# Kernel optimization log

Hardware: AMD Instinct MI355X
Metric: run time of the kernel (lower is better)

## Reference

```python
import jax, jax.numpy as jnp
import numpy as np

B, T, N, F_IN, F_OUT = 8, 16, 512, 128, 64
NEG_INF = -9e15


def setup_inputs() -> dict:
    key = jax.random.key(0)
    k1, k2, k3, k4, k5 = jax.random.split(key, 5)
    x = jax.random.normal(k1, (B, T, N, F_IN), dtype=jnp.float32)
    # nn.Linear weights: FC_W [out, in], FC_a [1, 2*out], no bias
    W = jax.random.normal(k2, (F_OUT, F_IN), dtype=jnp.float32) * 0.05
    a = jax.random.normal(k3, (1, 2 * F_OUT), dtype=jnp.float32) * 0.05
    adj = jax.random.randint(k4, (N, N), 0, 2, dtype=jnp.int32)
    adj_we = jax.random.uniform(k5, (N, N), dtype=jnp.float32)
    return {"x": x, "W": W, "a": a, "adj": adj, "adj_we": adj_we}


def reference(x, W, a, adj, adj_we):
    fout = W.shape[0]
    # h = FC_W(input): [B,T,N,Fout]
    h = jnp.einsum("btnf,of->btno", x, W)
    # Additive GAT score decomposition: e[i,j] = LeakyReLU(a1.h_i + a2.h_j)
    # (equivalent to FC_a(cat([h_i, h_j])) without materializing [B,T,N,N,2F])
    a1 = a[0, :fout]
    a2 = a[0, fout:]
    src = jnp.einsum("btno,o->btn", h, a1)  # contribution of node i (repeated rows)
    dst = jnp.einsum("btno,o->btn", h, a2)  # contribution of node j (tiled rows)
    e = jax.nn.leaky_relu(src[..., :, None] + dst[..., None, :], negative_slope=0.01)
    # mask where adj <= 0, scale by edge weights, softmax over neighbors (dim=3)
    att = jnp.where(adj > 0, e, NEG_INF)
    att = att * adj_we
    att = jax.nn.softmax(att, axis=-1)
    # h_prime = attention @ h : [B,T,N,N] @ [B,T,N,Fout]
    return jnp.einsum("btij,btjo->btio", att, h)
```

## Files before the change

### kernel.cpp

```cpp
#include <hip/hip_runtime.h>
#include <hip/hip_bf16.h>

#define BTOT 128
#define NN   512
#define FIN  128
#define FOUT 64

typedef __attribute__((ext_vector_type(8))) short bf16x8;
typedef __attribute__((ext_vector_type(4))) float f32x4;

static __device__ inline ushort f2bf(float f) {
    __hip_bfloat16 h = __float2bfloat16(f);
    return *(ushort*)&h;
}
static __device__ inline float bf2f(ushort u) {
    uint v = (uint)u << 16;
    return __uint_as_float(v);
}

__global__ void k_prep(const float* __restrict__ W, const int* __restrict__ adj,
                       const float* __restrict__ we, ushort* __restrict__ Whi,
                       ushort* __restrict__ Wlo, ushort* __restrict__ cds) {
    int b = blockIdx.x;
    if (b >= 256) {
        int i = (b - 256) * 256 + threadIdx.x;
        float w = W[i];
        ushort hi = f2bf(w);
        Whi[i] = hi;
        Wlo[i] = f2bf(w - bf2f(hi));
        return;
    }
    int i = (b * 256 + threadIdx.x) * 4;
    int4   a4 = *(const int4*)&adj[i];
    float4 w4 = *(const float4*)&we[i];
    ushort o[4];
#pragma unroll
    for (int e = 0; e < 4; ++e) {
        bool  cn = ((const int*)&a4)[e] > 0;
        float w  = ((const float*)&w4)[e];
        if (cn) {
            uint ub = __float_as_uint(w * 1.44269504f);
            uint tt = ub + 0xFFFFu + ((ub >> 17) & 1u);
            o[e] = (ushort)(((tt >> 17) << 1) | 1u);
        } else {
            o[e] = (w > 0.f) ? (ushort)0 : (ushort)1;
        }
    }
    *(uint2*)&cds[i] = *(uint2*)&o[0];
}

__global__ void k_feat(const float* __restrict__ x, const ushort* __restrict__ Whi,
                       const ushort* __restrict__ Wlo, const float* __restrict__ a,
                       ushort* __restrict__ ht, float* __restrict__ srcv,
                       float* __restrict__ dstv) {
    const int t    = threadIdx.x;
    const int bid  = blockIdx.x;
    const int bt   = bid & 127;
    const int nt   = bid >> 7;
    const int wv   = t >> 6, lane = t & 63;
    const int r    = lane & 15;
    const int kc   = lane >> 4;
    const int n0   = nt * 64 + wv * 16;

    const float* xrow = x + ((long)bt * NN + n0 + r) * FIN;

    f32x4 acc[4] = {{0,0,0,0},{0,0,0,0},{0,0,0,0},{0,0,0,0}};

#pragma unroll
    for (int ks = 0; ks < 4; ++ks) {
        f32x4 xa = __builtin_nontemporal_load((const f32x4*)&xrow[ks * 32 + kc * 8]);
        f32x4 xb = __builtin_nontemporal_load((const f32x4*)&xrow[ks * 32 + kc * 8 + 4]);
        float xv[8] = {xa[0], xa[1], xa[2], xa[3], xb[0], xb[1], xb[2], xb[3]};
        bf16x8 Ahi, Alo;
#pragma unroll
        for (int e = 0; e < 8; ++e) {
            uint b = __float_as_uint(xv[e]);
            float hf = __uint_as_float(b & 0xFFFF0000u);
            Ahi[e] = (short)(b >> 16);
            float rr = xv[e] - hf;
            Alo[e] = (short)(__float_as_uint(rr) >> 16);
        }
#pragma unroll
        for (int g = 0; g < 4; ++g) {
            const int wo = (g * 16 + r) * FIN + ks * 32 + kc * 8;
            bf16x8 Bhi = *(const bf16x8*)&Whi[wo];
            bf16x8 Blo = *(const bf16x8*)&Wlo[wo];
            acc[g] = __builtin_amdgcn_mfma_f32_16x16x32_bf16(Ahi, Bhi, acc[g], 0, 0, 0);
            acc[g] = __builtin_amdgcn_mfma_f32_16x16x32_bf16(Alo, Bhi, acc[g], 0, 0, 0);
            acc[g] = __builtin_amdgcn_mfma_f32_16x16x32_bf16(Ahi, Blo, acc[g], 0, 0, 0);
        }
    }

    float a1g[4], a2g[4];
#pragma unroll
    for (int g = 0; g < 4; ++g) {
        a1g[g] = a[g * 16 + r];
        a2g[g] = a[FOUT + g * 16 + r];
    }
    f32x4 s1v = {0,0,0,0}, s2v = {0,0,0,0};
#pragma unroll
    for (int g = 0; g < 4; ++g)
#pragma unroll
        for (int reg = 0; reg < 4; ++reg) {
            s1v[reg] += acc[g][reg] * a1g[g];
            s2v[reg] += acc[g][reg] * a2g[g];
        }
#pragma unroll
    for (int off = 8; off; off >>= 1)
#pragma unroll
        for (int reg = 0; reg < 4; ++reg) {
            s1v[reg] += __shfl_down(s1v[reg], off, 16);
            s2v[reg] += __shfl_down(s2v[reg], off, 16);
        }
    if (r == 0) {
        float4 o1 = make_float4(s1v[0], s1v[1], s1v[2], s1v[3]);
        float4 o2 = make_float4(s2v[0], s2v[1], s2v[2], s2v[3]);
        *(float4*)&srcv[bt * NN + n0 + kc * 4] = o1;
        *(float4*)&dstv[bt * NN + n0 + kc * 4] = o2;
    }

#pragma unroll
    for (int g = 0; g < 4; ++g) {
        uint2 pk;
        pk.x = (uint)f2bf(acc[g][0]) | ((uint)f2bf(acc[g][1]) << 16);
        pk.y = (uint)f2bf(acc[g][2]) | ((uint)f2bf(acc[g][3]) << 16);
        *(uint2*)&ht[(long)bt * (FOUT * NN) + (g * 16 + r) * NN + n0 + kc * 4] = pk;
    }
}

static __device__ inline bf16x8 make_afrag(uint4 c, float4 d0, float4 d1, float si) {
    float dv[8] = {d0.x, d0.y, d0.z, d0.w, d1.x, d1.y, d1.z, d1.w};
    uint  cw[4] = {c.x, c.y, c.z, c.w};
    union { uint u[4]; bf16x8 v; } A;
#pragma unroll
    for (int q = 0; q < 4; ++q) {
        uint u = cw[q];
        float c0 = __uint_as_float((u << 16) & 0xFFFE0000u);
        float c1 = __uint_as_float(u & 0xFFFE0000u);
        float s0 = si + dv[2 * q],     lr0 = fmaxf(s0, 0.01f * s0);
        float s1 = si + dv[2 * q + 1], lr1 = fmaxf(s1, 0.01f * s1);
        float p0 = __builtin_amdgcn_exp2f(c0 * lr0);
        float p1 = __builtin_amdgcn_exp2f(c1 * lr1);
        p0 = (u & 1u)       ? p0 : 0.f;
        p1 = (u & 0x10000u) ? p1 : 0.f;
        A.u[q] = __builtin_amdgcn_perm(__float_as_uint(p1), __float_as_uint(p0),
                                       0x07060302u);
    }
    return A.v;
}

__global__ __launch_bounds__(256, 4)
void k_attn(const ushort* __restrict__ ht, const float* __restrict__ srcv,
            const float* __restrict__ dstv, const ushort* __restrict__ cds,
            float* __restrict__ out) {
    __shared__ ushort hs[64 * 256];
    __shared__ float dst_s[NN];

    const int t    = threadIdx.x;
    const int bid  = blockIdx.x;
    const int bt   = bid & 127;
    const int i0   = (bid >> 7) << 6;
    const int lane = t & 63;
    const int wv   = t >> 6;
    const int r16  = lane & 15;
    const int kc   = lane >> 4;
    const int koff = kc * 8;
    const int xr   = r16 & 7;

    const int ri = i0 + wv * 16 + r16;
    const float si = srcv[bt * NN + ri];
    const ushort* cdr = cds + ri * NN;
    const ushort* htb = ht + (long)bt * (FOUT * NN);

    for (int q = t; q < NN; q += 256) dst_s[q] = dstv[bt * NN + q];

    f32x4 ac0 = {0,0,0,0}, ac1 = {0,0,0,0}, ac2 = {0,0,0,0}, ac3 = {0,0,0,0},
          acd = {0,0,0,0};
    bf16x8 ones;
#pragma unroll
    for (int j = 0; j < 8; ++j) ones[j] = (short)0x3F80;

#pragma unroll
    for (int half = 0; half < 2; ++half) {
        const int jg = half * 256;

        uint4 cdv[8];
#pragma unroll
        for (int c = 0; c < 4; ++c) {
            cdv[2 * c]     = *(const uint4*)&cdr[jg + c * 64 + koff];
            cdv[2 * c + 1] = *(const uint4*)&cdr[jg + c * 64 + 32 + koff];
        }

        __syncthreads();
#pragma unroll
        for (int q = 0; q < 8; ++q) {
            int idx = q * 256 + t;
            int o = idx >> 5, c8 = idx & 31;
            float4 v = *(const float4*)&htb[(o << 9) + (half << 8) + (c8 << 3)];
            *(float4*)&hs[(o << 8) + ((c8 ^ (o & 7)) << 3)] = v;
        }
        __syncthreads();

#pragma unroll
        for (int jtl = 0; jtl < 4; ++jtl) {
            const int jgc = jg + jtl * 64;
            float4 d00 = *(float4*)&dst_s[jgc + koff];
            float4 d01 = *(float4*)&dst_s[jgc + koff + 4];
            float4 d10 = *(float4*)&dst_s[jgc + 32 + koff];
            float4 d11 = *(float4*)&dst_s[jgc + 32 + koff + 4];

            bf16x8 A0 = make_afrag(cdv[2 * jtl],     d00, d01, si);
            bf16x8 A1 = make_afrag(cdv[2 * jtl + 1], d10, d11, si);

#pragma unroll
            for (int s2 = 0; s2 < 2; ++s2) {
                bf16x8 A = s2 ? A1 : A0;
                const int c8v = jtl * 8 + s2 * 4 + kc;
                const int cs  = (c8v ^ xr) << 3;
                bf16x8 b0 = *(bf16x8*)&hs[(( 0 + r16) << 8) + cs];
                bf16x8 b1 = *(bf16x8*)&hs[((16 + r16) << 8) + cs];
                bf16x8 b2 = *(bf16x8*)&hs[((32 + r16) << 8) + cs];
                bf16x8 b3 = *(bf16x8*)&hs[((48 + r16) << 8) + cs];
                __builtin_amdgcn_s_setprio(1);
                ac0 = __builtin_amdgcn_mfma_f32_16x16x32_bf16(A, b0, ac0, 0, 0, 0);
                ac1 = __builtin_amdgcn_mfma_f32_16x16x32_bf16(A, b1, ac1, 0, 0, 0);
                ac2 = __builtin_amdgcn_mfma_f32_16x16x32_bf16(A, b2, ac2, 0, 0, 0);
                ac3 = __builtin_amdgcn_mfma_f32_16x16x32_bf16(A, b3, ac3, 0, 0, 0);
                acd = __builtin_amdgcn_mfma_f32_16x16x32_bf16(A, ones, acd, 0, 0, 0);
                __builtin_amdgcn_s_setprio(0);
            }
        }
    }

    float* ob = out + ((long)bt * NN + i0 + wv * 16) * FOUT;
#pragma unroll
    for (int reg = 0; reg < 4; ++reg) {
        float inv = 1.0f / acd[reg];
        const int rw = (kc * 4 + reg) * FOUT + r16;
        __builtin_nontemporal_store(ac0[reg] * inv, &ob[rw +  0]);
        __builtin_nontemporal_store(ac1[reg] * inv, &ob[rw + 16]);
        __builtin_nontemporal_store(ac2[reg] * inv, &ob[rw + 32]);
        __builtin_nontemporal_store(ac3[reg] * inv, &ob[rw + 48]);
    }
}

extern "C" void kernel_launch(void* const* d_in, const int* in_sizes, int n_in,
                              void* d_out, int out_size, void* d_ws, size_t ws_size,
                              hipStream_t stream) {
    const float* x      = (const float*)d_in[0];
    const float* W      = (const float*)d_in[1];
    const float* a      = (const float*)d_in[2];
    const int*   adj    = (const int*)d_in[3];
    const float* adj_we = (const float*)d_in[4];
    float* out = (float*)d_out;

    ushort* Whi  = (ushort*)d_ws;
    ushort* Wlo  = Whi + FOUT * FIN;
    ushort* ht   = Wlo + FOUT * FIN;
    float*  srcv = (float*)(ht + BTOT * FOUT * NN);
    float*  dstv = srcv + BTOT * NN;
    ushort* cdsw = (ushort*)(dstv + BTOT * NN);

    hipLaunchKernelGGL(k_prep, dim3(288), dim3(256), 0, stream,
                       W, adj, adj_we, Whi, Wlo, cdsw);
    hipLaunchKernelGGL(k_feat, dim3(1024), dim3(256), 0, stream,
                       x, Whi, Wlo, a, ht, srcv, dstv);
    hipLaunchKernelGGL(k_attn, dim3(1024), dim3(256), 0, stream,
                       ht, srcv, dstv, cdsw, out);
}
```

Before: 48.36 us.

## Read attention B operands directly from global memory instead of LDS staging

Removes the shared-memory staging of the transposed h tile, along with its two barriers per half. Each wave now loads its MFMA B fragments straight from global or L2, and the cds row fragments are software-prefetched one chunk ahead. Launch bounds rise to 5 blocks per CU, since LDS use drops to just the dst vector. The trade-off is that the four waves of a block now fetch the same h data redundantly through cache instead of sharing it via LDS, and load latency is exposed directly on the MFMA path.

Result: slower. 70.88 us (+46.6%).

```diff
diff --git a/kernel.cpp b/kernel.cpp
--- a/kernel.cpp
+++ b/kernel.cpp
@@ -149,11 +149,10 @@
     return A.v;
 }
 
-__global__ __launch_bounds__(256, 4)
+__global__ __launch_bounds__(256, 5)
 void k_attn(const ushort* __restrict__ ht, const float* __restrict__ srcv,
             const float* __restrict__ dstv, const ushort* __restrict__ cds,
             float* __restrict__ out) {
-    __shared__ ushort hs[64 * 256];
     __shared__ float dst_s[NN];
 
     const int t    = threadIdx.x;
@@ -165,14 +164,18 @@
     const int r16  = lane & 15;
     const int kc   = lane >> 4;
     const int koff = kc * 8;
-    const int xr   = r16 & 7;
 
     const int ri = i0 + wv * 16 + r16;
     const float si = srcv[bt * NN + ri];
     const ushort* cdr = cds + ri * NN;
     const ushort* htb = ht + (long)bt * (FOUT * NN);
+    const ushort* hb0 = htb + ( 0 + r16) * NN;
+    const ushort* hb1 = htb + (16 + r16) * NN;
+    const ushort* hb2 = htb + (32 + r16) * NN;
+    const ushort* hb3 = htb + (48 + r16) * NN;
 
     for (int q = t; q < NN; q += 256) dst_s[q] = dstv[bt * NN + q];
+    __syncthreads();
 
     f32x4 ac0 = {0,0,0,0}, ac1 = {0,0,0,0}, ac2 = {0,0,0,0}, ac3 = {0,0,0,0},
           acd = {0,0,0,0};
@@ -180,55 +183,38 @@
 #pragma unroll
     for (int j = 0; j < 8; ++j) ones[j] = (short)0x3F80;
 
-#pragma unroll
-    for (int half = 0; half < 2; ++half) {
-        const int jg = half * 256;
-
-        uint4 cdv[8];
-#pragma unroll
-        for (int c = 0; c < 4; ++c) {
-            cdv[2 * c]     = *(const uint4*)&cdr[jg + c * 64 + koff];
-            cdv[2 * c + 1] = *(const uint4*)&cdr[jg + c * 64 + 32 + koff];
-        }
-
-        __syncthreads();
-#pragma unroll
-        for (int q = 0; q < 8; ++q) {
-            int idx = q * 256 + t;
-            int o = idx >> 5, c8 = idx & 31;
-            float4 v = *(const float4*)&htb[(o << 9) + (half << 8) + (c8 << 3)];
-            *(float4*)&hs[(o << 8) + ((c8 ^ (o & 7)) << 3)] = v;
-        }
-        __syncthreads();
-
-#pragma unroll
-        for (int jtl = 0; jtl < 4; ++jtl) {
-            const int jgc = jg + jtl * 64;
-            float4 d00 = *(float4*)&dst_s[jgc + koff];
-            float4 d01 = *(float4*)&dst_s[jgc + koff + 4];
-            float4 d10 = *(float4*)&dst_s[jgc + 32 + koff];
-            float4 d11 = *(float4*)&dst_s[jgc + 32 + koff + 4];
-
-            bf16x8 A0 = make_afrag(cdv[2 * jtl],     d00, d01, si);
-            bf16x8 A1 = make_afrag(cdv[2 * jtl + 1], d10, d11, si);
-
-#pragma unroll
-            for (int s2 = 0; s2 < 2; ++s2) {
-                bf16x8 A = s2 ? A1 : A0;
-                const int c8v = jtl * 8 + s2 * 4 + kc;
-                const int cs  = (c8v ^ xr) << 3;
-                bf16x8 b0 = *(bf16x8*)&hs[(( 0 + r16) << 8) + cs];
-                bf16x8 b1 = *(bf16x8*)&hs[((16 + r16) << 8) + cs];
-                bf16x8 b2 = *(bf16x8*)&hs[((32 + r16) << 8) + cs];
-                bf16x8 b3 = *(bf16x8*)&hs[((48 + r16) << 8) + cs];
-                __builtin_amdgcn_s_setprio(1);
-                ac0 = __builtin_amdgcn_mfma_f32_16x16x32_bf16(A, b0, ac0, 0, 0, 0);
-                ac1 = __builtin_amdgcn_mfma_f32_16x16x32_bf16(A, b1, ac1, 0, 0, 0);
-                ac2 = __builtin_amdgcn_mfma_f32_16x16x32_bf16(A, b2, ac2, 0, 0, 0);
-                ac3 = __builtin_amdgcn_mfma_f32_16x16x32_bf16(A, b3, ac3, 0, 0, 0);
-                acd = __builtin_amdgcn_mfma_f32_16x16x32_bf16(A, ones, acd, 0, 0, 0);
-                __builtin_amdgcn_s_setprio(0);
-            }
+    uint4 fA = *(const uint4*)&cdr[koff];
+    uint4 fB = *(const uint4*)&cdr[32 + koff];
+
+#pragma unroll
+    for (int ch = 0; ch < 8; ++ch) {
+        const int j0 = ch * 64;
+        uint4 cA = fA, cB = fB;
+        if (ch < 7) {
+            fA = *(const uint4*)&cdr[j0 + 64 + koff];
+            fB = *(const uint4*)&cdr[j0 + 96 + koff];
+        }
+        float4 d00 = *(float4*)&dst_s[j0 + koff];
+        float4 d01 = *(float4*)&dst_s[j0 + koff + 4];
+        float4 d10 = *(float4*)&dst_s[j0 + 32 + koff];
+        float4 d11 = *(float4*)&dst_s[j0 + 32 + koff + 4];
+
+        bf16x8 A0 = make_afrag(cA, d00, d01, si);
+        bf16x8 A1 = make_afrag(cB, d10, d11, si);
+
+#pragma unroll
+        for (int s2 = 0; s2 < 2; ++s2) {
+            bf16x8 A = s2 ? A1 : A0;
+            const int jb = j0 + s2 * 32 + koff;
+            bf16x8 b0 = *(const bf16x8*)&hb0[jb];
+            bf16x8 b1 = *(const bf16x8*)&hb1[jb];
+            bf16x8 b2 = *(const bf16x8*)&hb2[jb];
+            bf16x8 b3 = *(const bf16x8*)&hb3[jb];
+            ac0 = __builtin_amdgcn_mfma_f32_16x16x32_bf16(A, b0, ac0, 0, 0, 0);
+            ac1 = __builtin_amdgcn_mfma_f32_16x16x32_bf16(A, b1, ac1, 0, 0, 0);
+            ac2 = __builtin_amdgcn_mfma_f32_16x16x32_bf16(A, b2, ac2, 0, 0, 0);
+            ac3 = __builtin_amdgcn_mfma_f32_16x16x32_bf16(A, b3, ac3, 0, 0, 0);
+            acd = __builtin_amdgcn_mfma_f32_16x16x32_bf16(A, ones, acd, 0, 0, 0);
         }
     }
 
```

## Stage h tile through registers and build all A fragments before barrier

Applied to the files above, without the earlier changes.

The h tile loads into registers are issued together with the coefficient loads, and all eight softmax A fragments are computed before the first barrier. The tile is written to LDS afterwards, which overlaps global-load latency with the exp/leaky-relu math. The dst vector is read straight from global memory (cached) instead of being staged in LDS, and the MFMA loop runs under one raised-priority region. This raises register pressure (sreg plus afr arrays), which could reduce occupancy under the 256x4 launch bound.

Measured after the change: 65.91 us. 1.36x slower.

```diff
diff --git a/kernel.cpp b/kernel.cpp
--- a/kernel.cpp
+++ b/kernel.cpp
@@ -153,8 +153,7 @@
 void k_attn(const ushort* __restrict__ ht, const float* __restrict__ srcv,
             const float* __restrict__ dstv, const ushort* __restrict__ cds,
             float* __restrict__ out) {
-    __shared__ ushort hs[64 * 256];
-    __shared__ float dst_s[NN];
+    __shared__ ushort hs[FOUT * 256];
 
     const int t    = threadIdx.x;
     const int bid  = blockIdx.x;
@@ -169,10 +168,9 @@
 
     const int ri = i0 + wv * 16 + r16;
     const float si = srcv[bt * NN + ri];
-    const ushort* cdr = cds + ri * NN;
-    const ushort* htb = ht + (long)bt * (FOUT * NN);
-
-    for (int q = t; q < NN; q += 256) dst_s[q] = dstv[bt * NN + q];
+    const ushort* cdr  = cds + ri * NN;
+    const float*  dstr = dstv + bt * NN;
+    const ushort* htb  = ht + (long)bt * (FOUT * NN);
 
     f32x4 ac0 = {0,0,0,0}, ac1 = {0,0,0,0}, ac2 = {0,0,0,0}, ac3 = {0,0,0,0},
           acd = {0,0,0,0};
@@ -184,52 +182,51 @@
     for (int half = 0; half < 2; ++half) {
         const int jg = half * 256;
 
-        uint4 cdv[8];
-#pragma unroll
-        for (int c = 0; c < 4; ++c) {
-            cdv[2 * c]     = *(const uint4*)&cdr[jg + c * 64 + koff];
-            cdv[2 * c + 1] = *(const uint4*)&cdr[jg + c * 64 + 32 + koff];
-        }
-
-        __syncthreads();
+        float4 sreg[8];
 #pragma unroll
         for (int q = 0; q < 8; ++q) {
             int idx = q * 256 + t;
             int o = idx >> 5, c8 = idx & 31;
-            float4 v = *(const float4*)&htb[(o << 9) + (half << 8) + (c8 << 3)];
-            *(float4*)&hs[(o << 8) + ((c8 ^ (o & 7)) << 3)] = v;
-        }
+            sreg[q] = *(const float4*)&htb[(o << 9) + (half << 8) + (c8 << 3)];
+        }
+        uint4 cdv[8];
+#pragma unroll
+        for (int f = 0; f < 8; ++f)
+            cdv[f] = *(const uint4*)&cdr[jg + f * 32 + koff];
+
+        bf16x8 afr[8];
+#pragma unroll
+        for (int f = 0; f < 8; ++f) {
+            float4 d0 = *(const float4*)&dstr[jg + f * 32 + koff];
+            float4 d1 = *(const float4*)&dstr[jg + f * 32 + koff + 4];
+            afr[f] = make_afrag(cdv[f], d0, d1, si);
+        }
+
         __syncthreads();
-
-#pragma unroll
-        for (int jtl = 0; jtl < 4; ++jtl) {
-            const int jgc = jg + jtl * 64;
-            float4 d00 = *(float4*)&dst_s[jgc + koff];
-            float4 d01 = *(float4*)&dst_s[jgc + koff + 4];
-            float4 d10 = *(float4*)&dst_s[jgc + 32 + koff];
-            float4 d11 = *(float4*)&dst_s[jgc + 32 + koff + 4];
-
-            bf16x8 A0 = make_afrag(cdv[2 * jtl],     d00, d01, si);
-            bf16x8 A1 = make_afrag(cdv[2 * jtl + 1], d10, d11, si);
-
-#pragma unroll
-            for (int s2 = 0; s2 < 2; ++s2) {
-                bf16x8 A = s2 ? A1 : A0;
-                const int c8v = jtl * 8 + s2 * 4 + kc;
-                const int cs  = (c8v ^ xr) << 3;
-                bf16x8 b0 = *(bf16x8*)&hs[(( 0 + r16) << 8) + cs];
-                bf16x8 b1 = *(bf16x8*)&hs[((16 + r16) << 8) + cs];
-                bf16x8 b2 = *(bf16x8*)&hs[((32 + r16) << 8) + cs];
-                bf16x8 b3 = *(bf16x8*)&hs[((48 + r16) << 8) + cs];
-                __builtin_amdgcn_s_setprio(1);
-                ac0 = __builtin_amdgcn_mfma_f32_16x16x32_bf16(A, b0, ac0, 0, 0, 0);
-                ac1 = __builtin_amdgcn_mfma_f32_16x16x32_bf16(A, b1, ac1, 0, 0, 0);
-                ac2 = __builtin_amdgcn_mfma_f32_16x16x32_bf16(A, b2, ac2, 0, 0, 0);
-                ac3 = __builtin_amdgcn_mfma_f32_16x16x32_bf16(A, b3, ac3, 0, 0, 0);
-                acd = __builtin_amdgcn_mfma_f32_16x16x32_bf16(A, ones, acd, 0, 0, 0);
-                __builtin_amdgcn_s_setprio(0);
-            }
-        }
+#pragma unroll
+        for (int q = 0; q < 8; ++q) {
+            int idx = q * 256 + t;
+            int o = idx >> 5, c8 = idx & 31;
+            *(float4*)&hs[(o << 8) + ((c8 ^ (o & 7)) << 3)] = sreg[q];
+        }
+        __syncthreads();
+
+        __builtin_amdgcn_s_setprio(1);
+#pragma unroll
+        for (int f = 0; f < 8; ++f) {
+            const int cs = ((4 * f + kc) ^ xr) << 3;
+            bf16x8 b0 = *(bf16x8*)&hs[(( 0 + r16) << 8) + cs];
+            bf16x8 b1 = *(bf16x8*)&hs[((16 + r16) << 8) + cs];
+            bf16x8 b2 = *(bf16x8*)&hs[((32 + r16) << 8) + cs];
+            bf16x8 b3 = *(bf16x8*)&hs[((48 + r16) << 8) + cs];
+            bf16x8 A = afr[f];
+            ac0 = __builtin_amdgcn_mfma_f32_16x16x32_bf16(A, b0, ac0, 0, 0, 0);
+            ac1 = __builtin_amdgcn_mfma_f32_16x16x32_bf16(A, b1, ac1, 0, 0, 0);
+            ac2 = __builtin_amdgcn_mfma_f32_16x16x32_bf16(A, b2, ac2, 0, 0, 0);
+            ac3 = __builtin_amdgcn_mfma_f32_16x16x32_bf16(A, b3, ac3, 0, 0, 0);
+            acd = __builtin_amdgcn_mfma_f32_16x16x32_bf16(A, ones, acd, 0, 0, 0);
+        }
+        __builtin_amdgcn_s_setprio(0);
     }
 
     float* ob = out + ((long)bt * NN + i0 + wv * 16) * FOUT;
```
